# Performance work log

Measured on AMD Instinct MI355X. Metric: run time of the kernel, lower is better.

Reference implementation:

```python
import jax, jax.numpy as jnp
import numpy as np

N_NODES = 2_000_000
N_DAGS = 20_000
N_OBS = 1_000
DIM_EMBED = 32
NUM_NODE_FEATURES = 5
IN_DIM = NUM_NODE_FEATURES + 3 * DIM_EMBED  # 101
HIDDEN = [32, 16, 8, 1]


def _ragged_counts(rng, n_segments, total):
    # random nonnegative counts summing exactly to `total` (ragged partition)
    bounds = np.sort(rng.integers(0, total + 1, size=n_segments - 1))
    bounds = np.concatenate([[0], bounds, [total]])
    return jnp.asarray(np.diff(bounds), dtype=jnp.int64)


def setup_inputs() -> dict:
    key = jax.random.key(0)
    ks = jax.random.split(key, 16)
    rng = np.random.default_rng(0)

    inp = {
        "x": jax.random.normal(ks[0], (N_NODES, NUM_NODE_FEATURES), jnp.float32),
        "node_embeddings": jax.random.normal(ks[1], (N_NODES, DIM_EMBED), jnp.float32),
        "dag_summaries": jax.random.normal(ks[2], (N_DAGS, DIM_EMBED), jnp.float32),
        "global_summaries": jax.random.normal(ks[3], (N_OBS, DIM_EMBED), jnp.float32),
        "num_nodes_per_dag": _ragged_counts(rng, N_DAGS, N_NODES),
        "num_nodes_per_obs": _ragged_counts(rng, N_OBS, N_NODES),
        "stage_mask": jax.random.bernoulli(ks[4], 0.5, (N_NODES,)),
    }

    # MLP params: Linear(101,32) relu, Linear(32,16) relu, Linear(16,8) relu, Linear(8,1)
    dims = [IN_DIM] + HIDDEN
    for i in range(4):
        fan_in = dims[i]
        inp[f"W{i+1}"] = jax.random.normal(ks[5 + 2 * i], (dims[i], dims[i + 1]), jnp.float32) / np.sqrt(fan_in)
        inp[f"b{i+1}"] = jnp.zeros((dims[i + 1],), jnp.float32)
    return inp


def reference(x, node_embeddings, dag_summaries, global_summaries,
              num_nodes_per_dag, num_nodes_per_obs, stage_mask,
              W1, b1, W2, b2, W3, b3, W4, b4):
    n = x.shape[0]
    # ragged broadcast of per-dag / per-obs summaries to nodes
    dag_rep = jnp.repeat(dag_summaries, num_nodes_per_dag, axis=0, total_repeat_length=n)
    glob_rep = jnp.repeat(global_summaries, num_nodes_per_obs, axis=0, total_repeat_length=n)
    node_inputs = jnp.concatenate([x, node_embeddings, dag_rep, glob_rep], axis=1)  # [n, 101]

    h = jax.nn.relu(node_inputs @ W1 + b1)
    h = jax.nn.relu(h @ W2 + b2)
    h = jax.nn.relu(h @ W3 + b3)
    scores = (h @ W4 + b4)[:, 0]  # [n]

    min_real = jnp.finfo(scores.dtype).min
    return jax.nn.softmax(jnp.where(stage_mask, scores, min_real), axis=-1)
```

## Files before the change

kernel.cpp:

```cpp
#include <hip/hip_runtime.h>
#include <math.h>
#include <float.h>

#define BLK 256

__device__ __forceinline__ void scan_one(const int* __restrict__ cnt, int n,
                                         int* __restrict__ starts, int* wsum)
{
    const int t = threadIdx.x;
    const int chunk = (n + 1023) / 1024;
    const int base = t * chunk;

    int sum = 0;
    for (int k = 0; k < chunk; k++) {
        int idx = base + k;
        if (idx < n) sum += cnt[idx];
    }

    const int lane = t & 63, wid = t >> 6;
    int v = sum;
#pragma unroll
    for (int off = 1; off < 64; off <<= 1) {
        int y = __shfl_up(v, off);
        if (lane >= off) v += y;
    }
    if (lane == 63) wsum[wid] = v;
    __syncthreads();
    if (wid == 0) {
        int w = (lane < 16) ? wsum[lane] : 0;
#pragma unroll
        for (int off = 1; off < 16; off <<= 1) {
            int y = __shfl_up(w, off);
            if (lane >= off) w += y;
        }
        if (lane < 16) wsum[lane] = w;
    }
    __syncthreads();

    int thr_excl = ((wid > 0) ? wsum[wid - 1] : 0) + v - sum;
    int run = thr_excl;
    for (int k = 0; k < chunk; k++) {
        int idx = base + k;
        if (idx < n) { starts[idx] = run; run += cnt[idx]; }
    }
    if (t == 0) starts[n] = wsum[15];
    __syncthreads();
}

__global__ __launch_bounds__(1024) void scan2_kernel(
    const int* __restrict__ dag_cnt, int nd,
    const int* __restrict__ obs_cnt, int no,
    int* __restrict__ dag_starts, int* __restrict__ obs_starts)
{
    __shared__ int wsum[16];
    scan_one(dag_cnt, nd, dag_starts, wsum);
    scan_one(obs_cnt, no, obs_starts, wsum);
}

__global__ __launch_bounds__(128) void expand_ids_kernel(
    const int* __restrict__ dag_starts, int nd,
    const int* __restrict__ obs_starts, int no,
    int* __restrict__ dag_ids, int* __restrict__ obs_ids)
{
    int seg = blockIdx.x;
    if (seg < nd) {
        int s = dag_starts[seg], e = dag_starts[seg + 1];
        for (int i = s + threadIdx.x; i < e; i += 128) dag_ids[i] = seg;
    } else {
        int g = seg - nd;
        int s = obs_starts[g], e = obs_starts[g + 1];
        for (int i = s + threadIdx.x; i < e; i += 128) obs_ids[i] = g;
    }
}

__global__ __launch_bounds__(256) void seg_h1_kernel(
    const float* __restrict__ dag_sum, int nd,
    const float* __restrict__ glob_sum, int no,
    const float* __restrict__ W1, const float* __restrict__ b1,
    float* __restrict__ dag_h1, float* __restrict__ glob_h1)
{
    __shared__ float Wd[32 * 32];
    __shared__ float Wg[32 * 32];
    for (int t = threadIdx.x; t < 32 * 32; t += 256) {
        int k = t / 32, j = t % 32;
        Wd[t] = W1[(size_t)(37 + k) * 32 + j];
        Wg[t] = W1[(size_t)(69 + k) * 32 + j];
    }
    __syncthreads();

    int gid = blockIdx.x * 256 + threadIdx.x;
    int seg = gid / 32;
    int j   = gid % 32;
    if (seg >= nd + no) return;

    const float* srow;
    const float* Wl;
    float acc;
    float* outp;
    if (seg < nd) {
        srow = dag_sum + (size_t)seg * 32;
        Wl = Wd; acc = 0.f;
        outp = dag_h1 + (size_t)seg * 32 + j;
    } else {
        srow = glob_sum + (size_t)(seg - nd) * 32;
        Wl = Wg; acc = b1[j];
        outp = glob_h1 + (size_t)(seg - nd) * 32 + j;
    }
#pragma unroll
    for (int k = 0; k < 32; k++)
        acc = fmaf(srow[k], Wl[k * 32 + j], acc);
    *outp = acc;
}

__global__ __launch_bounds__(BLK) void mlp_score_kernel(
    const float* __restrict__ x, const float* __restrict__ emb,
    const float* __restrict__ dag_h1, const float* __restrict__ glob_h1,
    const int* __restrict__ dag_ids, const int* __restrict__ obs_ids,
    const int* __restrict__ mask,
    const float* __restrict__ W1, const float* __restrict__ W2,
    const float* __restrict__ b2, const float* __restrict__ W3,
    const float* __restrict__ b3, const float* __restrict__ W4,
    const float* __restrict__ b4,
    float* __restrict__ scores, float* __restrict__ blk_m,
    double* __restrict__ blk_s, int N)
{
    __shared__ float W1l[37 * 32];
    __shared__ float W2l[32 * 16];
    __shared__ float W3l[16 * 8];
    __shared__ float Cst[33];

    const int i0 = blockIdx.x * BLK + threadIdx.x;
    const bool valid = (i0 < N);
    const int i = valid ? i0 : (N - 1);

    const int d  = dag_ids[i];
    const int o  = obs_ids[i];
    const int mk = mask[i];
    const float* xr = x + (size_t)i * 5;
    float xv0 = xr[0], xv1 = xr[1], xv2 = xr[2], xv3 = xr[3], xv4 = xr[4];

    for (int t = threadIdx.x; t < 37 * 32; t += BLK) W1l[t] = W1[t];
    for (int t = threadIdx.x; t < 32 * 16; t += BLK) W2l[t] = W2[t];
    for (int t = threadIdx.x; t < 16 * 8;  t += BLK) W3l[t] = W3[t];
    if (threadIdx.x < 8)       Cst[threadIdx.x]      = W4[threadIdx.x];
    else if (threadIdx.x < 24) Cst[threadIdx.x]      = b2[threadIdx.x - 8];
    else if (threadIdx.x < 32) Cst[threadIdx.x]      = b3[threadIdx.x - 24];
    else if (threadIdx.x == 32) Cst[32]              = b4[0];
    __syncthreads();

    const float4* dh = (const float4*)(dag_h1 + (size_t)d * 32);
    const float4* gh = (const float4*)(glob_h1 + (size_t)o * 32);
    float4 dq0 = dh[0], dq1 = dh[1], dq2 = dh[2], dq3 = dh[3],
           dq4 = dh[4], dq5 = dh[5], dq6 = dh[6], dq7 = dh[7];
    float4 gq0 = gh[0], gq1 = gh[1], gq2 = gh[2], gq3 = gh[3],
           gq4 = gh[4], gq5 = gh[5], gq6 = gh[6], gq7 = gh[7];

    float h1[32];
#pragma unroll
    for (int j = 0; j < 32; j++) h1[j] = xv0 * W1l[j];
#pragma unroll
    for (int j = 0; j < 32; j++) h1[j] = fmaf(xv1, W1l[32 + j], h1[j]);
#pragma unroll
    for (int j = 0; j < 32; j++) h1[j] = fmaf(xv2, W1l[64 + j], h1[j]);
#pragma unroll
    for (int j = 0; j < 32; j++) h1[j] = fmaf(xv3, W1l[96 + j], h1[j]);
#pragma unroll
    for (int j = 0; j < 32; j++) h1[j] = fmaf(xv4, W1l[128 + j], h1[j]);

    const float4* er = (const float4*)(emb + (size_t)i * 32);
#pragma unroll
    for (int q = 0; q < 8; q++) {
        float4 e = er[q];
#pragma unroll
        for (int kk = 0; kk < 4; kk++) {
            const int k = 5 + q * 4 + kk;
            const float v = (kk == 0) ? e.x : (kk == 1) ? e.y : (kk == 2) ? e.z : e.w;
#pragma unroll
            for (int j = 0; j < 32; j++)
                h1[j] = fmaf(v, W1l[k * 32 + j], h1[j]);
        }
    }

#pragma unroll
    for (int c = 0; c < 4; c++) {
        h1[0  + c] += ((const float*)&dq0)[c] + ((const float*)&gq0)[c];
        h1[4  + c] += ((const float*)&dq1)[c] + ((const float*)&gq1)[c];
        h1[8  + c] += ((const float*)&dq2)[c] + ((const float*)&gq2)[c];
        h1[12 + c] += ((const float*)&dq3)[c] + ((const float*)&gq3)[c];
        h1[16 + c] += ((const float*)&dq4)[c] + ((const float*)&gq4)[c];
        h1[20 + c] += ((const float*)&dq5)[c] + ((const float*)&gq5)[c];
        h1[24 + c] += ((const float*)&dq6)[c] + ((const float*)&gq6)[c];
        h1[28 + c] += ((const float*)&dq7)[c] + ((const float*)&gq7)[c];
    }
#pragma unroll
    for (int j = 0; j < 32; j++) h1[j] = fmaxf(h1[j], 0.f);

    float h2[16];
#pragma unroll
    for (int j = 0; j < 16; j++) h2[j] = Cst[8 + j];
#pragma unroll
    for (int k = 0; k < 32; k++) {
        const float v = h1[k];
#pragma unroll
        for (int j = 0; j < 16; j++)
            h2[j] = fmaf(v, W2l[k * 16 + j], h2[j]);
    }
#pragma unroll
    for (int j = 0; j < 16; j++) h2[j] = fmaxf(h2[j], 0.f);

    float h3[8];
#pragma unroll
    for (int j = 0; j < 8; j++) h3[j] = Cst[24 + j];
#pragma unroll
    for (int k = 0; k < 16; k++) {
        const float v = h2[k];
#pragma unroll
        for (int j = 0; j < 8; j++)
            h3[j] = fmaf(v, W3l[k * 8 + j], h3[j]);
    }
#pragma unroll
    for (int j = 0; j < 8; j++) h3[j] = fmaxf(h3[j], 0.f);

    float s = Cst[32];
#pragma unroll
    for (int k = 0; k < 8; k++) s = fmaf(h3[k], Cst[k], s);

    const bool live = valid && (mk != 0);
    if (valid) scores[i0] = (mk != 0) ? s : -FLT_MAX;

    __shared__ float  mred[BLK];
    __shared__ double sred[BLK];
    mred[threadIdx.x] = live ? s : -INFINITY;
    sred[threadIdx.x] = live ? 1.0 : 0.0;
    __syncthreads();
    for (int off = BLK / 2; off > 0; off >>= 1) {
        if (threadIdx.x < off) {
            float ma = mred[threadIdx.x], mb = mred[threadIdx.x + off];
            double sa = sred[threadIdx.x], sb = sred[threadIdx.x + off];
            float M = fmaxf(ma, mb);
            double out = 0.0;
            if (ma > -INFINITY) out += sa * (double)expf(ma - M);
            if (mb > -INFINITY) out += sb * (double)expf(mb - M);
            mred[threadIdx.x] = M;
            sred[threadIdx.x] = out;
        }
        __syncthreads();
    }
    if (threadIdx.x == 0) {
        blk_m[blockIdx.x] = mred[0];
        blk_s[blockIdx.x] = sred[0];
    }
}

__global__ __launch_bounds__(1024) void merge_kernel(
    const float* __restrict__ bm, const double* __restrict__ bs, int n,
    float* __restrict__ gmax, double* __restrict__ Z)
{
    float m = -INFINITY;
    double s = 0.0;
    for (int i = threadIdx.x; i < n; i += 1024) {
        float mb = bm[i]; double sb = bs[i];
        float M = fmaxf(m, mb);
        double out = 0.0;
        if (m  > -INFINITY) out += s  * (double)expf(m  - M);
        if (mb > -INFINITY) out += sb * (double)expf(mb - M);
        m = M; s = out;
    }
    __shared__ float  mred[1024];
    __shared__ double sred[1024];
    mred[threadIdx.x] = m;
    sred[threadIdx.x] = s;
    __syncthreads();
    for (int off = 512; off > 0; off >>= 1) {
        if (threadIdx.x < off) {
            float ma = mred[threadIdx.x], mb = mred[threadIdx.x + off];
            double sa = sred[threadIdx.x], sb = sred[threadIdx.x + off];
            float M = fmaxf(ma, mb);
            double out = 0.0;
            if (ma > -INFINITY) out += sa * (double)expf(ma - M);
            if (mb > -INFINITY) out += sb * (double)expf(mb - M);
            mred[threadIdx.x] = M;
            sred[threadIdx.x] = out;
        }
        __syncthreads();
    }
    if (threadIdx.x == 0) { *gmax = mred[0]; *Z = sred[0]; }
}

__global__ __launch_bounds__(BLK) void finalize_kernel(
    const float* __restrict__ scores, int N,
    const float* __restrict__ gmaxp, const double* __restrict__ Zp,
    float* __restrict__ outp)
{
    const float gm = *gmaxp;
    const float rZ = (float)(1.0 / *Zp);
    int i = blockIdx.x * BLK + threadIdx.x;
    if (i < N) outp[i] = expf(scores[i] - gm) * rZ;
}

extern "C" void kernel_launch(void* const* d_in, const int* in_sizes, int n_in,
                              void* d_out, int out_size, void* d_ws, size_t ws_size,
                              hipStream_t stream)
{
    const float* x        = (const float*)d_in[0];
    const float* emb      = (const float*)d_in[1];
    const float* dag_sum  = (const float*)d_in[2];
    const float* glob_sum = (const float*)d_in[3];
    const int*   dag_cnt  = (const int*)d_in[4];
    const int*   obs_cnt  = (const int*)d_in[5];
    const int*   mask     = (const int*)d_in[6];
    const float* W1 = (const float*)d_in[7];
    const float* b1 = (const float*)d_in[8];
    const float* W2 = (const float*)d_in[9];
    const float* b2 = (const float*)d_in[10];
    const float* W3 = (const float*)d_in[11];
    const float* b3 = (const float*)d_in[12];
    const float* W4 = (const float*)d_in[13];
    const float* b4 = (const float*)d_in[14];
    float* outp = (float*)d_out;

    const int N  = in_sizes[0] / 5;
    const int nd = in_sizes[4];
    const int no = in_sizes[5];

    const int main_blocks = (N + BLK - 1) / BLK;

    char* ws = (char*)d_ws;
    size_t off = 0;
    auto alloc = [&](size_t bytes) {
        void* p = ws + off;
        off += (bytes + 15) & ~(size_t)15;
        return p;
    };
    int*    dag_starts = (int*)   alloc((size_t)(nd + 1) * sizeof(int));
    int*    obs_starts = (int*)   alloc((size_t)(no + 1) * sizeof(int));
    int*    dag_ids    = (int*)   alloc((size_t)N * sizeof(int));
    int*    obs_ids    = (int*)   alloc((size_t)N * sizeof(int));
    float*  dag_h1     = (float*) alloc((size_t)nd * 32 * sizeof(float));
    float*  glob_h1    = (float*) alloc((size_t)no * 32 * sizeof(float));
    float*  scores     = (float*) alloc((size_t)N * sizeof(float));
    float*  blk_m      = (float*) alloc((size_t)main_blocks * sizeof(float));
    double* blk_s      = (double*)alloc((size_t)main_blocks * sizeof(double));
    float*  gmax       = (float*) alloc(sizeof(float));
    double* Z          = (double*)alloc(sizeof(double));
    (void)ws_size;

    scan2_kernel<<<1, 1024, 0, stream>>>(dag_cnt, nd, obs_cnt, no, dag_starts, obs_starts);

    expand_ids_kernel<<<nd + no, 128, 0, stream>>>(dag_starts, nd, obs_starts, no, dag_ids, obs_ids);

    {
        int total = (nd + no) * 32;
        seg_h1_kernel<<<(total + 255) / 256, 256, 0, stream>>>(
            dag_sum, nd, glob_sum, no, W1, b1, dag_h1, glob_h1);
    }

    mlp_score_kernel<<<main_blocks, BLK, 0, stream>>>(
        x, emb, dag_h1, glob_h1, dag_ids, obs_ids, mask,
        W1, W2, b2, W3, b3, W4, b4, scores, blk_m, blk_s, N);

    merge_kernel<<<1, 1024, 0, stream>>>(blk_m, blk_s, main_blocks, gmax, Z);

    finalize_kernel<<<(N + BLK - 1) / BLK, BLK, 0, stream>>>(scores, N, gmax, Z, outp);
}
```

Measured before the change: 529.0 us.

## Read MLP weights directly from global memory and use wavefront shuffle reduction

Removes the per-block staging of W1/W2/W3 and biases into LDS along with its barrier, so weights are read straight from global memory as uniform (likely scalar-cached) loads. The block-level online-softmax reduction moves from a shared-memory tree with many barriers to wave64 shuffles plus a small cross-wave merge. The dag/global contributions now initialise h1 and the x/embedding loads are moved later. The risk is that weight reads which become scalar loads put more pressure on the scalar/constant cache, and double-precision shuffles cost extra instructions.

```diff
diff --git a/kernel.cpp b/kernel.cpp
--- a/kernel.cpp
+++ b/kernel.cpp
@@ -124,11 +124,6 @@
     float* __restrict__ scores, float* __restrict__ blk_m,
     double* __restrict__ blk_s, int N)
 {
-    __shared__ float W1l[37 * 32];
-    __shared__ float W2l[32 * 16];
-    __shared__ float W3l[16 * 8];
-    __shared__ float Cst[33];
-
     const int i0 = blockIdx.x * BLK + threadIdx.x;
     const bool valid = (i0 < N);
     const int i = valid ? i0 : (N - 1);
@@ -136,17 +131,6 @@
     const int d  = dag_ids[i];
     const int o  = obs_ids[i];
     const int mk = mask[i];
-    const float* xr = x + (size_t)i * 5;
-    float xv0 = xr[0], xv1 = xr[1], xv2 = xr[2], xv3 = xr[3], xv4 = xr[4];
-
-    for (int t = threadIdx.x; t < 37 * 32; t += BLK) W1l[t] = W1[t];
-    for (int t = threadIdx.x; t < 32 * 16; t += BLK) W2l[t] = W2[t];
-    for (int t = threadIdx.x; t < 16 * 8;  t += BLK) W3l[t] = W3[t];
-    if (threadIdx.x < 8)       Cst[threadIdx.x]      = W4[threadIdx.x];
-    else if (threadIdx.x < 24) Cst[threadIdx.x]      = b2[threadIdx.x - 8];
-    else if (threadIdx.x < 32) Cst[threadIdx.x]      = b3[threadIdx.x - 24];
-    else if (threadIdx.x == 32) Cst[32]              = b4[0];
-    __syncthreads();
 
     const float4* dh = (const float4*)(dag_h1 + (size_t)d * 32);
     const float4* gh = (const float4*)(glob_h1 + (size_t)o * 32);
@@ -155,19 +139,34 @@
     float4 gq0 = gh[0], gq1 = gh[1], gq2 = gh[2], gq3 = gh[3],
            gq4 = gh[4], gq5 = gh[5], gq6 = gh[6], gq7 = gh[7];
 
+    const float* xr = x + (size_t)i * 5;
+    float xv0 = xr[0], xv1 = xr[1], xv2 = xr[2], xv3 = xr[3], xv4 = xr[4];
+    const float4* er = (const float4*)(emb + (size_t)i * 32);
+
     float h1[32];
 #pragma unroll
-    for (int j = 0; j < 32; j++) h1[j] = xv0 * W1l[j];
-#pragma unroll
-    for (int j = 0; j < 32; j++) h1[j] = fmaf(xv1, W1l[32 + j], h1[j]);
-#pragma unroll
-    for (int j = 0; j < 32; j++) h1[j] = fmaf(xv2, W1l[64 + j], h1[j]);
-#pragma unroll
-    for (int j = 0; j < 32; j++) h1[j] = fmaf(xv3, W1l[96 + j], h1[j]);
-#pragma unroll
-    for (int j = 0; j < 32; j++) h1[j] = fmaf(xv4, W1l[128 + j], h1[j]);
-
-    const float4* er = (const float4*)(emb + (size_t)i * 32);
+    for (int c = 0; c < 4; c++) {
+        h1[0  + c] = ((const float*)&dq0)[c] + ((const float*)&gq0)[c];
+        h1[4  + c] = ((const float*)&dq1)[c] + ((const float*)&gq1)[c];
+        h1[8  + c] = ((const float*)&dq2)[c] + ((const float*)&gq2)[c];
+        h1[12 + c] = ((const float*)&dq3)[c] + ((const float*)&gq3)[c];
+        h1[16 + c] = ((const float*)&dq4)[c] + ((const float*)&gq4)[c];
+        h1[20 + c] = ((const float*)&dq5)[c] + ((const float*)&gq5)[c];
+        h1[24 + c] = ((const float*)&dq6)[c] + ((const float*)&gq6)[c];
+        h1[28 + c] = ((const float*)&dq7)[c] + ((const float*)&gq7)[c];
+    }
+
+#pragma unroll
+    for (int j = 0; j < 32; j++) h1[j] = fmaf(xv0, W1[j], h1[j]);
+#pragma unroll
+    for (int j = 0; j < 32; j++) h1[j] = fmaf(xv1, W1[32 + j], h1[j]);
+#pragma unroll
+    for (int j = 0; j < 32; j++) h1[j] = fmaf(xv2, W1[64 + j], h1[j]);
+#pragma unroll
+    for (int j = 0; j < 32; j++) h1[j] = fmaf(xv3, W1[96 + j], h1[j]);
+#pragma unroll
+    for (int j = 0; j < 32; j++) h1[j] = fmaf(xv4, W1[128 + j], h1[j]);
+
 #pragma unroll
     for (int q = 0; q < 8; q++) {
         float4 e = er[q];
@@ -177,78 +176,75 @@
             const float v = (kk == 0) ? e.x : (kk == 1) ? e.y : (kk == 2) ? e.z : e.w;
 #pragma unroll
             for (int j = 0; j < 32; j++)
-                h1[j] = fmaf(v, W1l[k * 32 + j], h1[j]);
+                h1[j] = fmaf(v, W1[k * 32 + j], h1[j]);
         }
     }
-
-#pragma unroll
-    for (int c = 0; c < 4; c++) {
-        h1[0  + c] += ((const float*)&dq0)[c] + ((const float*)&gq0)[c];
-        h1[4  + c] += ((const float*)&dq1)[c] + ((const float*)&gq1)[c];
-        h1[8  + c] += ((const float*)&dq2)[c] + ((const float*)&gq2)[c];
-        h1[12 + c] += ((const float*)&dq3)[c] + ((const float*)&gq3)[c];
-        h1[16 + c] += ((const float*)&dq4)[c] + ((const float*)&gq4)[c];
-        h1[20 + c] += ((const float*)&dq5)[c] + ((const float*)&gq5)[c];
-        h1[24 + c] += ((const float*)&dq6)[c] + ((const float*)&gq6)[c];
-        h1[28 + c] += ((const float*)&dq7)[c] + ((const float*)&gq7)[c];
-    }
 #pragma unroll
     for (int j = 0; j < 32; j++) h1[j] = fmaxf(h1[j], 0.f);
 
     float h2[16];
 #pragma unroll
-    for (int j = 0; j < 16; j++) h2[j] = Cst[8 + j];
+    for (int j = 0; j < 16; j++) h2[j] = b2[j];
 #pragma unroll
     for (int k = 0; k < 32; k++) {
         const float v = h1[k];
 #pragma unroll
         for (int j = 0; j < 16; j++)
-            h2[j] = fmaf(v, W2l[k * 16 + j], h2[j]);
+            h2[j] = fmaf(v, W2[k * 16 + j], h2[j]);
     }
 #pragma unroll
     for (int j = 0; j < 16; j++) h2[j] = fmaxf(h2[j], 0.f);
 
     float h3[8];
 #pragma unroll
-    for (int j = 0; j < 8; j++) h3[j] = Cst[24 + j];
+    for (int j = 0; j < 8; j++) h3[j] = b3[j];
 #pragma unroll
     for (int k = 0; k < 16; k++) {
         const float v = h2[k];
 #pragma unroll
         for (int j = 0; j < 8; j++)
-            h3[j] = fmaf(v, W3l[k * 8 + j], h3[j]);
+            h3[j] = fmaf(v, W3[k * 8 + j], h3[j]);
     }
 #pragma unroll
     for (int j = 0; j < 8; j++) h3[j] = fmaxf(h3[j], 0.f);
 
-    float s = Cst[32];
-#pragma unroll
-    for (int k = 0; k < 8; k++) s = fmaf(h3[k], Cst[k], s);
+    float s = b4[0];
+#pragma unroll
+    for (int k = 0; k < 8; k++) s = fmaf(h3[k], W4[k], s);
 
     const bool live = valid && (mk != 0);
-    if (valid) scores[i0] = (mk != 0) ? s : -FLT_MAX;
-
-    __shared__ float  mred[BLK];
-    __shared__ double sred[BLK];
-    mred[threadIdx.x] = live ? s : -INFINITY;
-    sred[threadIdx.x] = live ? 1.0 : 0.0;
-    __syncthreads();
-    for (int off = BLK / 2; off > 0; off >>= 1) {
-        if (threadIdx.x < off) {
-            float ma = mred[threadIdx.x], mb = mred[threadIdx.x + off];
-            double sa = sred[threadIdx.x], sb = sred[threadIdx.x + off];
-            float M = fmaxf(ma, mb);
+    if (valid) scores[i0] = live ? s : -FLT_MAX;
+
+    float  m  = live ? s : -INFINITY;
+    double sd = live ? 1.0 : 0.0;
+#pragma unroll
+    for (int off = 32; off > 0; off >>= 1) {
+        float  mo = __shfl_down(m, off);
+        double so = __shfl_down(sd, off);
+        float M = fmaxf(m, mo);
+        double out = 0.0;
+        if (m  > -INFINITY) out += sd * (double)expf(m  - M);
+        if (mo > -INFINITY) out += so * (double)expf(mo - M);
+        m = M; sd = out;
+    }
+    __shared__ float  mw[BLK / 64];
+    __shared__ double sw[BLK / 64];
+    const int lane = threadIdx.x & 63, wid = threadIdx.x >> 6;
+    if (lane == 0) { mw[wid] = m; sw[wid] = sd; }
+    __syncthreads();
+    if (threadIdx.x == 0) {
+        float M = mw[0]; double S = sw[0];
+#pragma unroll
+        for (int w = 1; w < BLK / 64; w++) {
+            float mb = mw[w]; double sb = sw[w];
+            float Mn = fmaxf(M, mb);
             double out = 0.0;
-            if (ma > -INFINITY) out += sa * (double)expf(ma - M);
-            if (mb > -INFINITY) out += sb * (double)expf(mb - M);
-            mred[threadIdx.x] = M;
-            sred[threadIdx.x] = out;
+            if (M  > -INFINITY) out += S  * (double)expf(M  - Mn);
+            if (mb > -INFINITY) out += sb * (double)expf(mb - Mn);
+            M = Mn; S = out;
         }
-        __syncthreads();
-    }
-    if (threadIdx.x == 0) {
-        blk_m[blockIdx.x] = mred[0];
-        blk_s[blockIdx.x] = sred[0];
+        blk_m[blockIdx.x] = M;
+        blk_s[blockIdx.x] = S;
     }
 }
 
```

New measurement: 493.3 us. 1.07x faster.
